# Kernel optimization log

Measured on AMD Instinct MI355X. Metric: run time of the kernel, lower is better.

## Reference

```python
import jax, jax.numpy as jnp
import numpy as np

IN_F = (16, 16, 16)
OUT_F = (16, 16, 16)
RANKS = (8, 8, 8, 8, 8, 8)


def setup_inputs() -> dict:
    key = jax.random.key(0)
    ks = jax.random.split(key, 9)
    x = jax.random.normal(ks[0], (4096, int(np.prod(IN_F))), dtype=jnp.float32)
    # core ~ U[0,1)*0.1 as in torch.rand(ranks)*0.1
    core = jax.random.uniform(ks[1], RANKS, dtype=jnp.float32) * 0.1
    # factor matrices: 3 out-side (out_f[i], r[i]) then 3 in-side (in_f[i], r[i+3])
    shapes = [(OUT_F[i], RANKS[i]) for i in range(3)] + [(IN_F[i], RANKS[i + 3]) for i in range(3)]
    f0, f1, f2, f3, f4, f5 = [
        jax.random.normal(ks[2 + i], shapes[i], dtype=jnp.float32) * 0.1 for i in range(6)
    ]
    bias = jnp.zeros((int(np.prod(OUT_F)),), dtype=jnp.float32)
    return {"x": x, "core": core, "f0": f0, "f1": f1, "f2": f2,
            "f3": f3, "f4": f4, "f5": f5, "bias": bias}


def reference(x, core, f0, f1, f2, f3, f4, f5, bias):
    # x: [N, prod(IN_F)] -> [N, i1, i2, i3]
    xr = x.reshape(-1, *IN_F)
    # Reconstruct full dense weight from Tucker factors (faithful to original)
    # core: [r0..r5]; f0..f2 out-side (out_dim, r); f3..f5 in-side (in_dim, r)
    W = jnp.einsum('ijklmn,ai,bj,ck,dl,em,fn->abcdef', core, f0, f1, f2, f3, f4, f5)
    # Contract input with in-side modes: [N, o1, o2, o3]
    res = jnp.einsum('abcdef,ndef->nabc', W, xr)
    y = res.reshape(-1, int(np.prod(OUT_F)))
    return y + bias
```

## Files before the change

### kernel.cpp

```cpp
#include <hip/hip_runtime.h>

#define THREADS 256

typedef __attribute__((ext_vector_type(8))) short bf16x8;
typedef __attribute__((ext_vector_type(4))) float f32x4;

__device__ inline unsigned short f2bf(float f) {
    union { float f; unsigned int u; } v; v.f = f;
    unsigned int r = v.u + 0x7fffu + ((v.u >> 16) & 1u);
    return (unsigned short)(r >> 16);
}

__device__ inline void lds_barrier() {
    asm volatile("s_waitcnt lgkmcnt(0)" ::: "memory");
    __builtin_amdgcn_s_barrier();
    __builtin_amdgcn_sched_barrier(0);
}

__global__ __launch_bounds__(THREADS) void k_in_contract(
    const float* __restrict__ x,
    const float* __restrict__ f3, const float* __restrict__ f4,
    const float* __restrict__ f5,
    unsigned short* __restrict__ u3b, int N)
{
    const int n = blockIdx.x;
    const int t = threadIdx.x;

    __shared__ float fs[256];
    __shared__ float u1s[256 * 9];
    __shared__ float u2s[128 * 9];

    if (t < 128) { fs[t] = f3[t]; fs[128 + t] = f4[t]; }

    float xv[16];
    {
        const float4* xr = (const float4*)(x + (size_t)n * 4096 + t * 16);
        float4 a0 = xr[0], a1 = xr[1], a2 = xr[2], a3 = xr[3];
        xv[0]=a0.x; xv[1]=a0.y; xv[2]=a0.z; xv[3]=a0.w;
        xv[4]=a1.x; xv[5]=a1.y; xv[6]=a1.z; xv[7]=a1.w;
        xv[8]=a2.x; xv[9]=a2.y; xv[10]=a2.z; xv[11]=a2.w;
        xv[12]=a3.x; xv[13]=a3.y; xv[14]=a3.z; xv[15]=a3.w;
    }

    float acc8[8];
    #pragma unroll
    for (int q = 0; q < 8; ++q) acc8[q] = 0.f;
    #pragma unroll
    for (int f = 0; f < 16; ++f) {
        const float xf = xv[f];
        #pragma unroll
        for (int n6 = 0; n6 < 8; ++n6)
            acc8[n6] = fmaf(xf, f5[f*8 + n6], acc8[n6]);
    }
    __syncthreads();
    #pragma unroll
    for (int n6 = 0; n6 < 8; ++n6) u1s[t*9 + n6] = acc8[n6];
    __syncthreads();

    {
        const int d = t >> 4, m = (t >> 1) & 7, h = t & 1;
        float fr[16];
        #pragma unroll
        for (int e = 0; e < 16; ++e) fr[e] = fs[128 + e*8 + m];
        float a4[4] = {0.f, 0.f, 0.f, 0.f};
        #pragma unroll
        for (int e = 0; e < 16; ++e) {
            const int base = (d*16 + e)*9 + h*4;
            #pragma unroll
            for (int q = 0; q < 4; ++q)
                a4[q] = fmaf(u1s[base + q], fr[e], a4[q]);
        }
        #pragma unroll
        for (int q = 0; q < 4; ++q) u2s[(d*8 + m)*9 + h*4 + q] = a4[q];
    }
    __syncthreads();

    {
        const int l = t >> 5, m = (t >> 2) & 7, h = t & 3;
        float fr[16];
        #pragma unroll
        for (int d = 0; d < 16; ++d) fr[d] = fs[d*8 + l];
        float a2[2] = {0.f, 0.f};
        #pragma unroll
        for (int d = 0; d < 16; ++d) {
            const int base = (d*8 + m)*9 + h*2;
            a2[0] = fmaf(u2s[base],     fr[d], a2[0]);
            a2[1] = fmaf(u2s[base + 1], fr[d], a2[1]);
        }
        unsigned int pk = (unsigned int)f2bf(a2[0]) |
                          ((unsigned int)f2bf(a2[1]) << 16);
        ((unsigned int*)u3b)[(size_t)n * 256 + t] = pk;
    }
}

__global__ __launch_bounds__(THREADS) void k_convert_core(
    const float* __restrict__ core, unsigned short* __restrict__ coreb)
{
    const int i = blockIdx.x * THREADS + threadIdx.x;
    float4 c = ((const float4*)core)[i];
    ushort4 o;
    o.x = f2bf(c.x); o.y = f2bf(c.y); o.z = f2bf(c.z); o.w = f2bf(c.w);
    ((ushort4*)coreb)[i] = o;
}

__global__ __launch_bounds__(THREADS) void k_core_gemm_mfma(
    const unsigned short* __restrict__ u3b,
    const unsigned short* __restrict__ coreb,
    float* __restrict__ v, int N)
{
    const int t    = threadIdx.x;
    const int lane = t & 63;
    const int wave = t >> 6;
    const int m0 = blockIdx.x * 128 + wave * 32;
    const int p0 = blockIdx.y * 32;
    const int lr = lane & 15;
    const int lq = lane >> 4;

    const unsigned short* aptr0 = u3b   + (size_t)(m0 + lr) * 512 + lq * 8;
    const unsigned short* aptr1 = aptr0 + 16 * 512;
    const unsigned short* bptr0 = coreb + (size_t)(p0 + lr) * 512 + lq * 8;
    const unsigned short* bptr1 = bptr0 + 16 * 512;

    f32x4 acc00 = {0.f,0.f,0.f,0.f}, acc01 = {0.f,0.f,0.f,0.f};
    f32x4 acc10 = {0.f,0.f,0.f,0.f}, acc11 = {0.f,0.f,0.f,0.f};

    #pragma unroll
    for (int k0 = 0; k0 < 512; k0 += 32) {
        bf16x8 a0 = *(const bf16x8*)(aptr0 + k0);
        bf16x8 a1 = *(const bf16x8*)(aptr1 + k0);
        bf16x8 b0 = *(const bf16x8*)(bptr0 + k0);
        bf16x8 b1 = *(const bf16x8*)(bptr1 + k0);
        acc00 = __builtin_amdgcn_mfma_f32_16x16x32_bf16(a0, b0, acc00, 0, 0, 0);
        acc01 = __builtin_amdgcn_mfma_f32_16x16x32_bf16(a0, b1, acc01, 0, 0, 0);
        acc10 = __builtin_amdgcn_mfma_f32_16x16x32_bf16(a1, b0, acc10, 0, 0, 0);
        acc11 = __builtin_amdgcn_mfma_f32_16x16x32_bf16(a1, b1, acc11, 0, 0, 0);
    }

    const int row = m0 + lq * 4;
    const int col = p0 + lr;
    #pragma unroll
    for (int r = 0; r < 4; ++r) {
        v[(size_t)(row + r) * 512 + col]           = acc00[r];
        v[(size_t)(row + r) * 512 + col + 16]      = acc01[r];
        v[(size_t)(row + 16 + r) * 512 + col]      = acc10[r];
        v[(size_t)(row + 16 + r) * 512 + col + 16] = acc11[r];
    }
}

__global__ __launch_bounds__(THREADS) void k_out_expand6(
    const float* __restrict__ v,
    const float* __restrict__ f0, const float* __restrict__ f1,
    const float* __restrict__ f2, const float* __restrict__ bias,
    float* __restrict__ y, int N)
{
    const int t  = threadIdx.x;
    const int r0 = blockIdx.x * 4;

    __shared__ float fs[256];
    __shared__ float vs[512];
    __shared__ float w1s[128 * 9];
    __shared__ float w2s[8 * 257];

    if (t < 128) { fs[t] = f0[t]; fs[128 + t] = f1[t]; }
    if (t < 128) ((float4*)vs)[t] = ((const float4*)(v + (size_t)r0 * 512))[t];

    float f2r[32];
    {
        const float4* fp = (const float4*)(f2 + ((t & 3) * 4) * 8);
        #pragma unroll
        for (int q8 = 0; q8 < 8; ++q8) {
            float4 ff = fp[q8];
            f2r[q8*4+0] = ff.x; f2r[q8*4+1] = ff.y;
            f2r[q8*4+2] = ff.z; f2r[q8*4+3] = ff.w;
        }
    }
    const float4* bias4 = (const float4*)bias;
    float4 bb0 = bias4[0*256 + t], bb1 = bias4[1*256 + t];
    float4 bb2 = bias4[2*256 + t], bb3 = bias4[3*256 + t];

    lds_barrier();

    const int a_ = t >> 4, j_ = (t >> 1) & 7, h_ = t & 1;
    const int b_ = t & 15;
    const int w_ = t >> 6, B_ = (t >> 2) & 15;

    float fr0[8], fr1[8];
    #pragma unroll
    for (int i = 0; i < 8; ++i) fr0[i] = fs[a_*8 + i];
    #pragma unroll
    for (int j = 0; j < 8; ++j) fr1[j] = fs[128 + b_*8 + j];

    #pragma unroll 1
    for (int rr = 0; rr < 4; ++rr) {
        const int n = r0 + rr;

        float4 vpf = make_float4(0.f, 0.f, 0.f, 0.f);
        if (rr < 3 && t < 128)
            vpf = ((const float4*)(v + (size_t)(n + 1) * 512))[t];

        {
            float a4[4] = {0.f, 0.f, 0.f, 0.f};
            #pragma unroll
            for (int i = 0; i < 8; ++i) {
                const int base = i*64 + j_*8 + h_*4;
                const float fi = fr0[i];
                #pragma unroll
                for (int q = 0; q < 4; ++q)
                    a4[q] = fmaf(vs[base + q], fi, a4[q]);
            }
            #pragma unroll
            for (int q = 0; q < 4; ++q) w1s[(a_*8 + j_)*9 + h_*4 + q] = a4[q];
        }
        lds_barrier();

        {
            float w2[8] = {0.f,0.f,0.f,0.f,0.f,0.f,0.f,0.f};
            #pragma unroll
            for (int j = 0; j < 8; ++j) {
                const int base = (a_*8 + j)*9;
                const float fj = fr1[j];
                #pragma unroll
                for (int k = 0; k < 8; ++k)
                    w2[k] = fmaf(w1s[base + k], fj, w2[k]);
            }
            #pragma unroll
            for (int k = 0; k < 8; ++k) w2s[k*257 + t] = w2[k];
        }
        if (rr < 3 && t < 128) ((float4*)vs)[t] = vpf;
        lds_barrier();

        {
            float4* y4 = (float4*)(y + (size_t)n * 4096);
            #pragma unroll
            for (int s = 0; s < 4; ++s) {
                const int AB = (s*4 + w_) * 16 + B_;
                float w2v[8];
                #pragma unroll
                for (int k = 0; k < 8; ++k) w2v[k] = w2s[k*257 + AB];

                float4 bb = (s == 0) ? bb0 : (s == 1) ? bb1
                          : (s == 2) ? bb2 : bb3;
                float rv0 = bb.x, rv1 = bb.y, rv2 = bb.z, rv3 = bb.w;
                #pragma unroll
                for (int k = 0; k < 8; ++k) {
                    rv0 = fmaf(w2v[k], f2r[0*8 + k], rv0);
                    rv1 = fmaf(w2v[k], f2r[1*8 + k], rv1);
                    rv2 = fmaf(w2v[k], f2r[2*8 + k], rv2);
                    rv3 = fmaf(w2v[k], f2r[3*8 + k], rv3);
                }
                y4[s*256 + t] = make_float4(rv0, rv1, rv2, rv3);
            }
        }
        lds_barrier();
    }
}

extern "C" void kernel_launch(void* const* d_in, const int* in_sizes, int n_in,
                              void* d_out, int out_size, void* d_ws, size_t ws_size,
                              hipStream_t stream)
{
    const float* x    = (const float*)d_in[0];
    const float* core = (const float*)d_in[1];
    const float* f0   = (const float*)d_in[2];
    const float* f1   = (const float*)d_in[3];
    const float* f2   = (const float*)d_in[4];
    const float* f3   = (const float*)d_in[5];
    const float* f4   = (const float*)d_in[6];
    const float* f5   = (const float*)d_in[7];
    const float* bias = (const float*)d_in[8];
    float* y = (float*)d_out;

    const int N = in_sizes[0] / 4096;

    unsigned short* u3b   = (unsigned short*)d_ws;
    unsigned short* coreb = u3b + (size_t)N * 512;
    float*          v     = (float*)(coreb + 512 * 512);

    k_in_contract<<<N, THREADS, 0, stream>>>(x, f3, f4, f5, u3b, N);
    k_convert_core<<<256, THREADS, 0, stream>>>(core, coreb);
    dim3 gb(N / 128, 512 / 32);
    k_core_gemm_mfma<<<gb, THREADS, 0, stream>>>(u3b, coreb, v, N);
    k_out_expand6<<<N / 4, THREADS, 0, stream>>>(v, f0, f1, f2, bias, y, N);
}
```

Measured before the change: 153.3 us.

## Fuse second and third contraction stages, double-buffer LDS to cut barriers

The out-expand kernel no longer stages the f1-contracted intermediate in shared memory. Each thread now recomputes its w2 values directly from double-buffered w1s rows with float4 reads, then applies f2. Ping-pong buffers for vs and w1s reduce the barriers per row from three to one, and the row loop is fully unrolled. In exchange, the f1 contraction is done redundantly by the threads sharing a row, and the kernel uses more LDS and registers.

```diff
diff --git a/kernel.cpp b/kernel.cpp
--- a/kernel.cpp
+++ b/kernel.cpp
@@ -147,7 +147,7 @@
     }
 }
 
-__global__ __launch_bounds__(THREADS) void k_out_expand6(
+__global__ __launch_bounds__(THREADS) void k_out_expand7(
     const float* __restrict__ v,
     const float* __restrict__ f0, const float* __restrict__ f1,
     const float* __restrict__ f2, const float* __restrict__ bias,
@@ -157,12 +157,12 @@
     const int r0 = blockIdx.x * 4;
 
     __shared__ float fs[256];
-    __shared__ float vs[512];
-    __shared__ float w1s[128 * 9];
-    __shared__ float w2s[8 * 257];
+    __shared__ float vs[2][512];
+    __shared__ float w1s[2][128 * 12];
 
     if (t < 128) { fs[t] = f0[t]; fs[128 + t] = f1[t]; }
-    if (t < 128) ((float4*)vs)[t] = ((const float4*)(v + (size_t)r0 * 512))[t];
+    if (t < 128)
+        ((float4*)&vs[0][0])[t] = ((const float4*)(v + (size_t)r0 * 512))[t];
 
     float f2r[32];
     {
@@ -178,21 +178,21 @@
     float4 bb0 = bias4[0*256 + t], bb1 = bias4[1*256 + t];
     float4 bb2 = bias4[2*256 + t], bb3 = bias4[3*256 + t];
 
+    const int a_ = t >> 4, j_ = (t >> 1) & 7, h_ = t & 1;
+    const int w_ = t >> 6, B_ = (t >> 2) & 15;
+
     lds_barrier();
 
-    const int a_ = t >> 4, j_ = (t >> 1) & 7, h_ = t & 1;
-    const int b_ = t & 15;
-    const int w_ = t >> 6, B_ = (t >> 2) & 15;
-
     float fr0[8], fr1[8];
     #pragma unroll
     for (int i = 0; i < 8; ++i) fr0[i] = fs[a_*8 + i];
     #pragma unroll
-    for (int j = 0; j < 8; ++j) fr1[j] = fs[128 + b_*8 + j];
-
-    #pragma unroll 1
+    for (int j = 0; j < 8; ++j) fr1[j] = fs[128 + B_*8 + j];
+
+    #pragma unroll
     for (int rr = 0; rr < 4; ++rr) {
         const int n = r0 + rr;
+        const int p = rr & 1;
 
         float4 vpf = make_float4(0.f, 0.f, 0.f, 0.f);
         if (rr < 3 && t < 128)
@@ -206,38 +206,36 @@
                 const float fi = fr0[i];
                 #pragma unroll
                 for (int q = 0; q < 4; ++q)
-                    a4[q] = fmaf(vs[base + q], fi, a4[q]);
+                    a4[q] = fmaf(vs[p][base + q], fi, a4[q]);
             }
-            #pragma unroll
-            for (int q = 0; q < 4; ++q) w1s[(a_*8 + j_)*9 + h_*4 + q] = a4[q];
-        }
-        lds_barrier();
-
-        {
-            float w2[8] = {0.f,0.f,0.f,0.f,0.f,0.f,0.f,0.f};
-            #pragma unroll
-            for (int j = 0; j < 8; ++j) {
-                const int base = (a_*8 + j)*9;
-                const float fj = fr1[j];
-                #pragma unroll
-                for (int k = 0; k < 8; ++k)
-                    w2[k] = fmaf(w1s[base + k], fj, w2[k]);
-            }
-            #pragma unroll
-            for (int k = 0; k < 8; ++k) w2s[k*257 + t] = w2[k];
-        }
-        if (rr < 3 && t < 128) ((float4*)vs)[t] = vpf;
+            *(float4*)&w1s[p][(a_*8 + j_)*12 + h_*4] =
+                make_float4(a4[0], a4[1], a4[2], a4[3]);
+        }
+        if (rr < 3 && t < 128) ((float4*)&vs[p ^ 1][0])[t] = vpf;
+
         lds_barrier();
 
         {
             float4* y4 = (float4*)(y + (size_t)n * 4096);
             #pragma unroll
             for (int s = 0; s < 4; ++s) {
-                const int AB = (s*4 + w_) * 16 + B_;
-                float w2v[8];
+                const int A = s*4 + w_;
+                float w2v[8] = {0.f,0.f,0.f,0.f,0.f,0.f,0.f,0.f};
                 #pragma unroll
-                for (int k = 0; k < 8; ++k) w2v[k] = w2s[k*257 + AB];
-
+                for (int j = 0; j < 8; ++j) {
+                    const int wb = (A*8 + j) * 12;
+                    float4 wlo = *(const float4*)&w1s[p][wb];
+                    float4 whi = *(const float4*)&w1s[p][wb + 4];
+                    const float fj = fr1[j];
+                    w2v[0] = fmaf(wlo.x, fj, w2v[0]);
+                    w2v[1] = fmaf(wlo.y, fj, w2v[1]);
+                    w2v[2] = fmaf(wlo.z, fj, w2v[2]);
+                    w2v[3] = fmaf(wlo.w, fj, w2v[3]);
+                    w2v[4] = fmaf(whi.x, fj, w2v[4]);
+                    w2v[5] = fmaf(whi.y, fj, w2v[5]);
+                    w2v[6] = fmaf(whi.z, fj, w2v[6]);
+                    w2v[7] = fmaf(whi.w, fj, w2v[7]);
+                }
                 float4 bb = (s == 0) ? bb0 : (s == 1) ? bb1
                           : (s == 2) ? bb2 : bb3;
                 float rv0 = bb.x, rv1 = bb.y, rv2 = bb.z, rv3 = bb.w;
@@ -251,7 +249,6 @@
                 y4[s*256 + t] = make_float4(rv0, rv1, rv2, rv3);
             }
         }
-        lds_barrier();
     }
 }
 
@@ -280,5 +277,5 @@
     k_convert_core<<<256, THREADS, 0, stream>>>(core, coreb);
     dim3 gb(N / 128, 512 / 32);
     k_core_gemm_mfma<<<gb, THREADS, 0, stream>>>(u3b, coreb, v, N);
-    k_out_expand6<<<N / 4, THREADS, 0, stream>>>(v, f0, f1, f2, bias, y, N);
-}
+    k_out_expand7<<<N / 4, THREADS, 0, stream>>>(v, f0, f1, f2, bias, y, N);
+}
```

Measured after the change: 156.1 us. Within noise of the previous version (+1.8%).

## Process four rows per block in input contraction with prefetch and double-buffered LDS

Applied to the files above, without the earlier changes.

The input-side contraction kernel now handles four rows per block instead of one. It prefetches the next row of x while computing the current one, and alternates two LDS buffers so one barrier can be dropped per stage. Factor loads from LDS are hoisted out of the row loop. This cuts per-block setup and launch overhead and hides global load latency, but the grid drops to N/4 blocks, which lowers parallelism and raises register and LDS use.

```diff
diff --git a/kernel.cpp b/kernel.cpp
--- a/kernel.cpp
+++ b/kernel.cpp
@@ -17,79 +17,97 @@
     __builtin_amdgcn_sched_barrier(0);
 }
 
-__global__ __launch_bounds__(THREADS) void k_in_contract(
+__global__ __launch_bounds__(THREADS) void k_in_contract8(
     const float* __restrict__ x,
     const float* __restrict__ f3, const float* __restrict__ f4,
     const float* __restrict__ f5,
     unsigned short* __restrict__ u3b, int N)
 {
-    const int n = blockIdx.x;
-    const int t = threadIdx.x;
+    const int t  = threadIdx.x;
+    const int r0 = blockIdx.x * 4;
 
     __shared__ float fs[256];
-    __shared__ float u1s[256 * 9];
-    __shared__ float u2s[128 * 9];
+    __shared__ float u1s[2][256 * 9];
+    __shared__ float u2s[2][128 * 9];
 
     if (t < 128) { fs[t] = f3[t]; fs[128 + t] = f4[t]; }
 
-    float xv[16];
+    const int d2 = t >> 4, m2 = (t >> 1) & 7, h2 = t & 1;
+    const int l3 = t >> 5, m3 = (t >> 2) & 7, h3 = t & 3;
+
+    float4 xc0, xc1, xc2, xc3;
     {
-        const float4* xr = (const float4*)(x + (size_t)n * 4096 + t * 16);
-        float4 a0 = xr[0], a1 = xr[1], a2 = xr[2], a3 = xr[3];
-        xv[0]=a0.x; xv[1]=a0.y; xv[2]=a0.z; xv[3]=a0.w;
-        xv[4]=a1.x; xv[5]=a1.y; xv[6]=a1.z; xv[7]=a1.w;
-        xv[8]=a2.x; xv[9]=a2.y; xv[10]=a2.z; xv[11]=a2.w;
-        xv[12]=a3.x; xv[13]=a3.y; xv[14]=a3.z; xv[15]=a3.w;
-    }
-
-    float acc8[8];
-    #pragma unroll
-    for (int q = 0; q < 8; ++q) acc8[q] = 0.f;
-    #pragma unroll
-    for (int f = 0; f < 16; ++f) {
-        const float xf = xv[f];
-        #pragma unroll
-        for (int n6 = 0; n6 < 8; ++n6)
-            acc8[n6] = fmaf(xf, f5[f*8 + n6], acc8[n6]);
-    }
-    __syncthreads();
-    #pragma unroll
-    for (int n6 = 0; n6 < 8; ++n6) u1s[t*9 + n6] = acc8[n6];
-    __syncthreads();
-
-    {
-        const int d = t >> 4, m = (t >> 1) & 7, h = t & 1;
-        float fr[16];
-        #pragma unroll
-        for (int e = 0; e < 16; ++e) fr[e] = fs[128 + e*8 + m];
-        float a4[4] = {0.f, 0.f, 0.f, 0.f};
-        #pragma unroll
-        for (int e = 0; e < 16; ++e) {
-            const int base = (d*16 + e)*9 + h*4;
+        const float4* xr = (const float4*)(x + (size_t)r0 * 4096 + t * 16);
+        xc0 = xr[0]; xc1 = xr[1]; xc2 = xr[2]; xc3 = xr[3];
+    }
+
+    lds_barrier();
+
+    float fr4[16], fr3[16];
+    #pragma unroll
+    for (int e = 0; e < 16; ++e) fr4[e] = fs[128 + e*8 + m2];
+    #pragma unroll
+    for (int d = 0; d < 16; ++d) fr3[d] = fs[d*8 + l3];
+
+    #pragma unroll
+    for (int rr = 0; rr < 4; ++rr) {
+        const int n = r0 + rr;
+        const int p = rr & 1;
+
+        float4 xn0, xn1, xn2, xn3;
+        if (rr < 3) {
+            const float4* xr = (const float4*)(x + (size_t)(n + 1) * 4096 + t * 16);
+            xn0 = xr[0]; xn1 = xr[1]; xn2 = xr[2]; xn3 = xr[3];
+        }
+
+        {
+            float xv[16] = {xc0.x,xc0.y,xc0.z,xc0.w, xc1.x,xc1.y,xc1.z,xc1.w,
+                            xc2.x,xc2.y,xc2.z,xc2.w, xc3.x,xc3.y,xc3.z,xc3.w};
+            float acc8[8];
+            #pragma unroll
+            for (int q = 0; q < 8; ++q) acc8[q] = 0.f;
+            #pragma unroll
+            for (int f = 0; f < 16; ++f) {
+                const float xf = xv[f];
+                #pragma unroll
+                for (int n6 = 0; n6 < 8; ++n6)
+                    acc8[n6] = fmaf(xf, f5[f*8 + n6], acc8[n6]);
+            }
+            #pragma unroll
+            for (int n6 = 0; n6 < 8; ++n6) u1s[p][t*9 + n6] = acc8[n6];
+        }
+        lds_barrier();
+
+        {
+            float a4[4] = {0.f, 0.f, 0.f, 0.f};
+            #pragma unroll
+            for (int e = 0; e < 16; ++e) {
+                const int base = (d2*16 + e)*9 + h2*4;
+                const float fe = fr4[e];
+                #pragma unroll
+                for (int q = 0; q < 4; ++q)
+                    a4[q] = fmaf(u1s[p][base + q], fe, a4[q]);
+            }
             #pragma unroll
             for (int q = 0; q < 4; ++q)
-                a4[q] = fmaf(u1s[base + q], fr[e], a4[q]);
-        }
-        #pragma unroll
-        for (int q = 0; q < 4; ++q) u2s[(d*8 + m)*9 + h*4 + q] = a4[q];
-    }
-    __syncthreads();
-
-    {
-        const int l = t >> 5, m = (t >> 2) & 7, h = t & 3;
-        float fr[16];
-        #pragma unroll
-        for (int d = 0; d < 16; ++d) fr[d] = fs[d*8 + l];
-        float a2[2] = {0.f, 0.f};
-        #pragma unroll
-        for (int d = 0; d < 16; ++d) {
-            const int base = (d*8 + m)*9 + h*2;
-            a2[0] = fmaf(u2s[base],     fr[d], a2[0]);
-            a2[1] = fmaf(u2s[base + 1], fr[d], a2[1]);
-        }
-        unsigned int pk = (unsigned int)f2bf(a2[0]) |
-                          ((unsigned int)f2bf(a2[1]) << 16);
-        ((unsigned int*)u3b)[(size_t)n * 256 + t] = pk;
+                u2s[p][(d2*8 + m2)*9 + h2*4 + q] = a4[q];
+        }
+        lds_barrier();
+
+        {
+            float a2[2] = {0.f, 0.f};
+            #pragma unroll
+            for (int d = 0; d < 16; ++d) {
+                const int base = (d*8 + m3)*9 + h3*2;
+                a2[0] = fmaf(u2s[p][base],     fr3[d], a2[0]);
+                a2[1] = fmaf(u2s[p][base + 1], fr3[d], a2[1]);
+            }
+            unsigned int pk = (unsigned int)f2bf(a2[0]) |
+                              ((unsigned int)f2bf(a2[1]) << 16);
+            ((unsigned int*)u3b)[(size_t)n * 256 + t] = pk;
+        }
+
+        if (rr < 3) { xc0 = xn0; xc1 = xn1; xc2 = xn2; xc3 = xn3; }
     }
 }
 
@@ -276,7 +294,7 @@
     unsigned short* coreb = u3b + (size_t)N * 512;
     float*          v     = (float*)(coreb + 512 * 512);
 
-    k_in_contract<<<N, THREADS, 0, stream>>>(x, f3, f4, f5, u3b, N);
+    k_in_contract8<<<N / 4, THREADS, 0, stream>>>(x, f3, f4, f5, u3b, N);
     k_convert_core<<<256, THREADS, 0, stream>>>(core, coreb);
     dim3 gb(N / 128, 512 / 32);
     k_core_gemm_mfma<<<gb, THREADS, 0, stream>>>(u3b, coreb, v, N);
```

Result: no change. 153.7 us (+0.2%).
